# Kernel tuning notes

Hardware: AMD Instinct MI355X
Metric: run time of the kernel (lower is better)

Reference implementation:

```python
import jax, jax.numpy as jnp
import numpy as np

HIDDEN = 768
NUM_HEADS = 12
HEAD_DIM = HIDDEN // NUM_HEADS


def setup_inputs() -> dict:
    key = jax.random.key(0)
    ks = jax.random.split(key, 10)
    B, S = 4, 2048
    scale = 1.0 / np.sqrt(HIDDEN)
    inp = {
        "hidden_states": jax.random.normal(ks[0], (B, S, HIDDEN), dtype=jnp.float32),
        "attention_mask": jnp.ones((B, S), dtype=jnp.float32),
        "Wq": jax.random.normal(ks[1], (HIDDEN, HIDDEN), dtype=jnp.float32) * scale,
        "bq": jnp.zeros((HIDDEN,), dtype=jnp.float32),
        "Wk": jax.random.normal(ks[2], (HIDDEN, HIDDEN), dtype=jnp.float32) * scale,
        "bk": jnp.zeros((HIDDEN,), dtype=jnp.float32),
        "Wv": jax.random.normal(ks[3], (HIDDEN, HIDDEN), dtype=jnp.float32) * scale,
        "bv": jnp.zeros((HIDDEN,), dtype=jnp.float32),
        "Wo": jax.random.normal(ks[4], (HIDDEN, HIDDEN), dtype=jnp.float32) * scale,
        "bo": jnp.zeros((HIDDEN,), dtype=jnp.float32),
    }
    return inp


def _split_heads(x):
    # [B,S,H] -> [B,nh,S,dh]
    B, S, _ = x.shape
    return x.reshape(B, S, NUM_HEADS, HEAD_DIM).transpose(0, 2, 1, 3)


def reference(hidden_states, attention_mask, Wq, bq, Wk, bk, Wv, bv, Wo, bo):
    # Linear projections (torch nn.Linear: x @ W.T + b; here W stored as [in,out])
    q = _split_heads(hidden_states @ Wq + bq)
    k = _split_heads(hidden_states @ Wk + bk)
    v = _split_heads(hidden_states @ Wv + bv)

    # scores: [B,nh,S,S]
    scores = jnp.einsum("bhqd,bhkd->bhqk", q, k) / np.sqrt(HEAD_DIM).astype(np.float32)

    # outer-product mask: [B,1,S,S], broadcast over heads
    ext = (attention_mask[:, :, None] * attention_mask[:, None, :])[:, None, :, :]
    scores = ext * scores - (1.0 - ext) * 1e9

    probs = jax.nn.softmax(scores, axis=-1)
    ctx = jnp.einsum("bhqk,bhkd->bhqd", probs, v)  # [B,nh,S,dh]
    B, _, S, _ = ctx.shape
    ctx = ctx.transpose(0, 2, 1, 3).reshape(B, S, HIDDEN)
    out = ctx @ Wo + bo
    # torch F.gelu default: exact (erf-based)
    return jax.nn.gelu(out, approximate=False)
```

## Files before the change

### kernel.cpp

```cpp
#include <hip/hip_runtime.h>
#include <math.h>

#define HIDDEN 768
#define NH 12
#define DH 64
#define SEQ 2048
#define BATCH 4

typedef __bf16 bf16;
typedef bf16 bf16x4 __attribute__((ext_vector_type(4)));
typedef bf16 bf16x8 __attribute__((ext_vector_type(8)));
typedef float f32x4 __attribute__((ext_vector_type(4)));

__device__ __forceinline__ void load_lds16(const void* g, void* l) {
    __builtin_amdgcn_global_load_lds(
        (__attribute__((address_space(1))) void*)g,
        (__attribute__((address_space(3))) void*)l, 16, 0, 0);
}

__global__ __launch_bounds__(256) void prep_x(const float* __restrict__ X,
                                              bf16* __restrict__ Xb) {
    const size_t i = ((size_t)blockIdx.x * 256 + threadIdx.x) * 8;
    float4 a = *(const float4*)(X + i);
    float4 b = *(const float4*)(X + i + 4);
    bf16x8 o = {(bf16)a.x, (bf16)a.y, (bf16)a.z, (bf16)a.w,
                (bf16)b.x, (bf16)b.y, (bf16)b.z, (bf16)b.w};
    *(bf16x8*)(Xb + i) = o;
}

__global__ __launch_bounds__(256) void prep_w(const float* __restrict__ Wq,
                                              const float* __restrict__ Wk,
                                              const float* __restrict__ Wv,
                                              const float* __restrict__ Wo,
                                              bf16* __restrict__ Wt,
                                              bf16* __restrict__ Wot_hi,
                                              bf16* __restrict__ Wot_lo) {
    __shared__ float Ts[64][68];
    const int tid = threadIdx.x;
    const int n0 = blockIdx.x * 64, k0 = blockIdx.y * 64, z = blockIdx.z;
    const float* W = (z == 0) ? Wq : (z == 1) ? Wk : (z == 2) ? Wv : Wo;

    {
        const int r = tid >> 2, c = (tid & 3) << 4;
        const float* src = W + (size_t)(k0 + r) * HIDDEN + n0 + c;
#pragma unroll
        for (int j = 0; j < 4; ++j)
            *(float4*)&Ts[r][c + 4 * j] = *(const float4*)(src + 4 * j);
    }
    __syncthreads();

    const int nl = tid >> 2, kc = (tid & 3) << 4;
    float v[16];
#pragma unroll
    for (int j = 0; j < 16; ++j) v[j] = Ts[kc + j][nl];

    if (z < 3) {
        bf16 hi[16];
#pragma unroll
        for (int j = 0; j < 16; ++j) hi[j] = (bf16)v[j];
        const size_t off = (size_t)(z * HIDDEN + n0 + nl) * HIDDEN + k0 + kc;
        *(bf16x8*)(Wt + off) = *(bf16x8*)&hi[0];
        *(bf16x8*)(Wt + off + 8) = *(bf16x8*)&hi[8];
    } else {
        bf16 hi[16], lo[16];
#pragma unroll
        for (int j = 0; j < 16; ++j) {
            hi[j] = (bf16)v[j];
            lo[j] = (bf16)(v[j] - (float)hi[j]);
        }
        const size_t off = (size_t)(n0 + nl) * HIDDEN + k0 + kc;
        *(bf16x8*)(Wot_hi + off) = *(bf16x8*)&hi[0];
        *(bf16x8*)(Wot_hi + off + 8) = *(bf16x8*)&hi[8];
        *(bf16x8*)(Wot_lo + off) = *(bf16x8*)&lo[0];
        *(bf16x8*)(Wot_lo + off + 8) = *(bf16x8*)&lo[8];
    }
}

__global__ __launch_bounds__(256, 3) void gemm_qkv(
    const bf16* __restrict__ Xb, const bf16* __restrict__ Wt,
    const float* __restrict__ bq, const float* __restrict__ bk,
    const float* __restrict__ bv, bf16* __restrict__ q_out,
    bf16* __restrict__ k_out, bf16* __restrict__ v_out) {
    __shared__ bf16 As[128 * 64];
    __shared__ bf16 Bs[192 * 64];

    const int tid = threadIdx.x;
    const int ln = tid & 63, wv = tid >> 6;
    const int quad = ln >> 4, l16 = ln & 15;
    const int wm = wv >> 1, wn = wv & 1;
    const int n0 = blockIdx.x * 192, m0 = blockIdx.y * 128;

    f32x4 acc[4][6];
#pragma unroll
    for (int i = 0; i < 4; ++i)
#pragma unroll
        for (int j = 0; j < 6; ++j) acc[i][j] = (f32x4){0.f, 0.f, 0.f, 0.f};

    const int r8 = ln >> 3;
    const int bcol_sw = ((ln & 7) << 4) ^ (r8 << 4);
    const char* gA =
        (const char*)Xb + ((size_t)(m0 + wv * 32 + r8) * HIDDEN) * 2 + bcol_sw;
    const char* gB =
        (const char*)Wt + ((size_t)(n0 + wv * 48 + r8) * HIDDEN) * 2 + bcol_sw;
    bf16* As_w = As + (wv * 32) * 64;
    bf16* Bs_w = Bs + (wv * 48) * 64;

    const int fsw = (l16 & 7) << 4;

    for (int k0 = 0; k0 < HIDDEN; k0 += 64) {
        __syncthreads();
#pragma unroll
        for (int j = 0; j < 4; ++j)
            load_lds16(gA + (size_t)k0 * 2 + (size_t)j * (8 * HIDDEN * 2),
                       As_w + j * 8 * 64);
#pragma unroll
        for (int j = 0; j < 6; ++j)
            load_lds16(gB + (size_t)k0 * 2 + (size_t)j * (8 * HIDDEN * 2),
                       Bs_w + j * 8 * 64);
        __syncthreads();

#pragma unroll
        for (int kk = 0; kk < 2; ++kk) {
            const int kb = kk * 64;
            bf16x8 ah[4], bh[6];
#pragma unroll
            for (int i = 0; i < 4; ++i)
                ah[i] = *(const bf16x8*)((const char*)As +
                                         (wm * 64 + i * 16 + l16) * 128 +
                                         ((kb + quad * 16) ^ fsw));
#pragma unroll
            for (int i = 0; i < 6; ++i)
                bh[i] = *(const bf16x8*)((const char*)Bs +
                                         (wn * 96 + i * 16 + l16) * 128 +
                                         ((kb + quad * 16) ^ fsw));
#pragma unroll
            for (int mi = 0; mi < 4; ++mi)
#pragma unroll
                for (int ni = 0; ni < 6; ++ni)
                    acc[mi][ni] = __builtin_amdgcn_mfma_f32_16x16x32_bf16(
                        ah[mi], bh[ni], acc[mi][ni], 0, 0, 0);
        }
    }

    const int nb = n0 + wn * 96;
    const int which = nb / HIDDEN;
    const int nrel = nb - which * HIDDEN;

    if (which < 2) {
        const float scale = (which == 0) ? 0.18033688011112042f : 1.0f;
        const float* bias = (which == 0) ? bq : bk;
        bf16* dst = (which == 0) ? q_out : k_out;
#pragma unroll
        for (int ni = 0; ni < 6; ++ni) {
            const int nn = nrel + ni * 16;
            const int h = nn >> 6;
            const int dh = (nn & 63) + l16;
            const float bb = bias[nn + l16];
#pragma unroll
            for (int mi = 0; mi < 4; ++mi)
#pragma unroll
                for (int r = 0; r < 4; ++r) {
                    const int m = m0 + wm * 64 + mi * 16 + quad * 4 + r;
                    const int bi = m >> 11, s = m & (SEQ - 1);
                    dst[(((size_t)(bi * NH + h) * SEQ + s) << 6) + dh] =
                        (bf16)(scale * (acc[mi][ni][r] + bb));
                }
        }
    } else {
        const int bi = m0 >> 11;
        const int sbase = (m0 & (SEQ - 1)) + wm * 64;
#pragma unroll
        for (int ni = 0; ni < 6; ++ni) {
            const int nn = nrel + ni * 16;
            const int h = nn >> 6;
            const int dh = (nn & 63) + l16;
            const float bb = bv[nn + l16];
            bf16* vrow = v_out + ((size_t)(bi * NH + h) * DH + dh) * SEQ;
#pragma unroll
            for (int mi = 0; mi < 4; ++mi) {
                bf16x4 pk = {(bf16)(acc[mi][ni][0] + bb),
                             (bf16)(acc[mi][ni][1] + bb),
                             (bf16)(acc[mi][ni][2] + bb),
                             (bf16)(acc[mi][ni][3] + bb)};
                *(bf16x4*)(vrow + sbase + mi * 16 + quad * 4) = pk;
            }
        }
    }
}

__global__ __launch_bounds__(256) void attn_mfma(const bf16* __restrict__ Q,
                                                 const bf16* __restrict__ K,
                                                 const bf16* __restrict__ Vt,
                                                 const float* __restrict__ mask,
                                                 bf16* __restrict__ ctx_hi,
                                                 bf16* __restrict__ ctx_lo) {
    __shared__ bf16 Ks[64 * 64];
    __shared__ bf16 Vts[64 * 64];
    __shared__ bf16 Ps[128 * 64];
    __shared__ float Ms[SEQ];
    __shared__ int allones_s;

    const int tid = threadIdx.x;
    const int ln = tid & 63, w = tid >> 6;
    const int quad = ln >> 4, l16 = ln & 15;

    const int wg = blockIdx.x;
    const int logical = (wg & 7) * 96 + (wg >> 3);
    const int qt = logical & 15;
    const int h = (logical >> 4) % NH;
    const int b = logical / (16 * NH);

    const size_t bh = (size_t)b * NH + h;
    const bf16* Qp = Q + ((bh * SEQ + (size_t)qt * 128) << 6);
    const bf16* Kp = K + (bh * SEQ << 6);
    const bf16* Vp = Vt + (bh * DH) * SEQ;

    if (tid == 0) allones_s = 1;
    {
        float4 m0 = *(const float4*)(mask + (size_t)b * SEQ + tid * 8);
        float4 m1 = *(const float4*)(mask + (size_t)b * SEQ + tid * 8 + 4);
        *(float4*)&Ms[tid * 8] = m0;
        *(float4*)&Ms[tid * 8 + 4] = m1;
        bool ok = (m0.x == 1.f) & (m0.y == 1.f) & (m0.z == 1.f) &
                  (m0.w == 1.f) & (m1.x == 1.f) & (m1.y == 1.f) &
                  (m1.z == 1.f) & (m1.w == 1.f);
        __syncthreads();
        if (!ok) allones_s = 0;
    }
    __syncthreads();
    const bool fastmask = (allones_s != 0);

    bf16x8 qb[2][2];
#pragma unroll
    for (int qg = 0; qg < 2; ++qg)
#pragma unroll
        for (int hf = 0; hf < 2; ++hf)
            qb[qg][hf] = *(const bf16x8*)(Qp + ((w * 32 + qg * 16 + l16) << 6) +
                                          hf * 32 + quad * 8);
    float mq[2];
#pragma unroll
    for (int qg = 0; qg < 2; ++qg)
        mq[qg] = Ms[qt * 128 + w * 32 + qg * 16 + l16];

    float l_i[2] = {0.f, 0.f};
    f32x4 acc[4][2];
#pragma unroll
    for (int fd = 0; fd < 4; ++fd)
#pragma unroll
        for (int qg = 0; qg < 2; ++qg) acc[fd][qg] = (f32x4){0.f, 0.f, 0.f, 0.f};

    const int sr = tid >> 2, sc = (tid & 3) << 4;
    const int ssw = (sr & 7) << 3;
    const int d0 = sc ^ ssw, d1 = (sc + 8) ^ ssw;
    const bf16* kbase = Kp + ((size_t)sr << 6) + sc;
    const bf16* vbase = Vp + (size_t)sr * SEQ + sc;

    bf16x8 kr0, kr1, vr0, vr1;
    kr0 = *(const bf16x8*)kbase;
    kr1 = *(const bf16x8*)(kbase + 8);
    vr0 = *(const bf16x8*)vbase;
    vr1 = *(const bf16x8*)(vbase + 8);

    for (int kt = 0; kt < SEQ / 64; ++kt) {
        __syncthreads();
        *(bf16x8*)&Ks[sr * 64 + d0] = kr0;
        *(bf16x8*)&Ks[sr * 64 + d1] = kr1;
        *(bf16x8*)&Vts[sr * 64 + d0] = vr0;
        *(bf16x8*)&Vts[sr * 64 + d1] = vr1;
        __syncthreads();
        if (kt + 1 < SEQ / 64) {
            kr0 = *(const bf16x8*)(kbase + ((size_t)(kt + 1) << 12));
            kr1 = *(const bf16x8*)(kbase + ((size_t)(kt + 1) << 12) + 8);
            vr0 = *(const bf16x8*)(vbase + (kt + 1) * 64);
            vr1 = *(const bf16x8*)(vbase + (kt + 1) * 64 + 8);
        }

        const int fsw = (l16 & 7) << 3;
        f32x4 st[4][2];
#pragma unroll
        for (int f = 0; f < 4; ++f) {
            const int krow = (f * 16 + l16) * 64;
            bf16x8 ka0 = *(bf16x8*)&Ks[krow + ((quad * 8) ^ fsw)];
            bf16x8 ka1 = *(bf16x8*)&Ks[krow + ((32 + quad * 8) ^ fsw)];
#pragma unroll
            for (int qg = 0; qg < 2; ++qg) {
                f32x4 c = {0.f, 0.f, 0.f, 0.f};
                c = __builtin_amdgcn_mfma_f32_16x16x32_bf16(ka0, qb[qg][0], c, 0, 0, 0);
                c = __builtin_amdgcn_mfma_f32_16x16x32_bf16(ka1, qb[qg][1], c, 0, 0, 0);
                st[f][qg] = c;
            }
        }

        if (!fastmask) {
#pragma unroll
            for (int f = 0; f < 4; ++f) {
                const float4 mk4 = *(const float4*)&Ms[kt * 64 + f * 16 + quad * 4];
                const float mkk[4] = {mk4.x, mk4.y, mk4.z, mk4.w};
#pragma unroll
                for (int qg = 0; qg < 2; ++qg)
#pragma unroll
                    for (int r = 0; r < 4; ++r) {
                        const float ext = mq[qg] * mkk[r];
                        st[f][qg][r] =
                            ext * st[f][qg][r] - (1.0f - ext) * 1.4426950e9f;
                    }
            }
        }

#pragma unroll
        for (int qg = 0; qg < 2; ++qg) {
            const int row = w * 32 + qg * 16 + l16;
            const int sw = (row & 7) << 3;
            bf16* prow = &Ps[row * 64];
#pragma unroll
            for (int f = 0; f < 4; ++f) {
                float p0 = __builtin_amdgcn_exp2f(st[f][qg][0]);
                float p1 = __builtin_amdgcn_exp2f(st[f][qg][1]);
                float p2 = __builtin_amdgcn_exp2f(st[f][qg][2]);
                float p3 = __builtin_amdgcn_exp2f(st[f][qg][3]);
                l_i[qg] += (p0 + p1) + (p2 + p3);
                bf16x4 pk = {(bf16)p0, (bf16)p1, (bf16)p2, (bf16)p3};
                *(bf16x4*)&prow[(f * 16 + quad * 4) ^ sw] = pk;
            }
        }

        bf16x8 pb[2][2];
#pragma unroll
        for (int qg = 0; qg < 2; ++qg) {
            const int row = w * 32 + qg * 16 + l16;
            const int sw = (row & 7) << 3;
#pragma unroll
            for (int hf = 0; hf < 2; ++hf)
                pb[qg][hf] =
                    *(bf16x8*)&Ps[row * 64 + ((hf * 32 + quad * 8) ^ sw)];
        }
#pragma unroll
        for (int fd = 0; fd < 4; ++fd) {
            const int vrow = (fd * 16 + l16) * 64;
            bf16x8 va0 = *(bf16x8*)&Vts[vrow + ((quad * 8) ^ fsw)];
            bf16x8 va1 = *(bf16x8*)&Vts[vrow + ((32 + quad * 8) ^ fsw)];
#pragma unroll
            for (int qg = 0; qg < 2; ++qg) {
                f32x4 c = acc[fd][qg];
                c = __builtin_amdgcn_mfma_f32_16x16x32_bf16(va0, pb[qg][0], c, 0, 0, 0);
                c = __builtin_amdgcn_mfma_f32_16x16x32_bf16(va1, pb[qg][1], c, 0, 0, 0);
                acc[fd][qg] = c;
            }
        }
    }

#pragma unroll
    for (int qg = 0; qg < 2; ++qg) {
        l_i[qg] += __shfl_xor(l_i[qg], 16);
        l_i[qg] += __shfl_xor(l_i[qg], 32);
    }

#pragma unroll
    for (int qg = 0; qg < 2; ++qg) {
        const float inv = 1.0f / l_i[qg];
        const size_t row = (size_t)b * SEQ + qt * 128 + w * 32 + qg * 16 + l16;
#pragma unroll
        for (int fd = 0; fd < 4; ++fd) {
            bf16 hi[4], lo[4];
#pragma unroll
            for (int r = 0; r < 4; ++r) {
                const float o = acc[fd][qg][r] * inv;
                hi[r] = (bf16)o;
                lo[r] = (bf16)(o - (float)hi[r]);
            }
            const size_t off = row * HIDDEN + h * 64 + fd * 16 + quad * 4;
            *(bf16x4*)(ctx_hi + off) = *(bf16x4*)&hi[0];
            *(bf16x4*)(ctx_lo + off) = *(bf16x4*)&lo[0];
        }
    }
}

__global__ __launch_bounds__(256) void gemm_out(const bf16* __restrict__ Ah,
                                                const bf16* __restrict__ Al,
                                                const bf16* __restrict__ Bhi,
                                                const bf16* __restrict__ Blo,
                                                const float* __restrict__ bo,
                                                float* __restrict__ fout) {
    __shared__ bf16 As_hi[128 * 64];
    __shared__ bf16 As_lo[128 * 64];
    __shared__ bf16 Bs_hi[64 * 64];
    __shared__ bf16 Bs_lo[64 * 64];

    const int tid = threadIdx.x;
    const int ln = tid & 63, wv = tid >> 6;
    const int quad = ln >> 4, l16 = ln & 15;
    const int wm = wv >> 1, wn = wv & 1;
    const int n0 = blockIdx.x * 64, m0 = blockIdx.y * 128;

    f32x4 acc[4][2];
#pragma unroll
    for (int i = 0; i < 4; ++i)
#pragma unroll
        for (int j = 0; j < 2; ++j) acc[i][j] = (f32x4){0.f, 0.f, 0.f, 0.f};

    const int r8 = ln >> 3;
    const int bcol_sw = ((ln & 7) << 4) ^ (r8 << 4);
    const char* gAh =
        (const char*)Ah + ((size_t)(m0 + wv * 32 + r8) * HIDDEN) * 2 + bcol_sw;
    const char* gAl =
        (const char*)Al + ((size_t)(m0 + wv * 32 + r8) * HIDDEN) * 2 + bcol_sw;
    const char* gBh =
        (const char*)Bhi + ((size_t)(n0 + wv * 16 + r8) * HIDDEN) * 2 + bcol_sw;
    const char* gBl =
        (const char*)Blo + ((size_t)(n0 + wv * 16 + r8) * HIDDEN) * 2 + bcol_sw;
    bf16* Ash_w = As_hi + (wv * 32) * 64;
    bf16* Asl_w = As_lo + (wv * 32) * 64;
    bf16* Bsh_w = Bs_hi + (wv * 16) * 64;
    bf16* Bsl_w = Bs_lo + (wv * 16) * 64;

    const int fsw = (l16 & 7) << 4;

    for (int k0 = 0; k0 < HIDDEN; k0 += 64) {
        __syncthreads();
#pragma unroll
        for (int j = 0; j < 4; ++j) {
            load_lds16(gAh + (size_t)k0 * 2 + (size_t)j * (8 * HIDDEN * 2),
                       Ash_w + j * 8 * 64);
            load_lds16(gAl + (size_t)k0 * 2 + (size_t)j * (8 * HIDDEN * 2),
                       Asl_w + j * 8 * 64);
        }
#pragma unroll
        for (int j = 0; j < 2; ++j) {
            load_lds16(gBh + (size_t)k0 * 2 + (size_t)j * (8 * HIDDEN * 2),
                       Bsh_w + j * 8 * 64);
            load_lds16(gBl + (size_t)k0 * 2 + (size_t)j * (8 * HIDDEN * 2),
                       Bsl_w + j * 8 * 64);
        }
        __syncthreads();

#pragma unroll
        for (int kk = 0; kk < 2; ++kk) {
            const int kb = kk * 64;
            bf16x8 ah[4], al[4], bh[2], bl[2];
#pragma unroll
            for (int i = 0; i < 4; ++i) {
                const int row = (wm * 64 + i * 16 + l16) * 128;
                ah[i] = *(const bf16x8*)((const char*)As_hi + row +
                                         ((kb + quad * 16) ^ fsw));
                al[i] = *(const bf16x8*)((const char*)As_lo + row +
                                         ((kb + quad * 16) ^ fsw));
            }
#pragma unroll
            for (int i = 0; i < 2; ++i) {
                const int row = (wn * 32 + i * 16 + l16) * 128;
                bh[i] = *(const bf16x8*)((const char*)Bs_hi + row +
                                         ((kb + quad * 16) ^ fsw));
                bl[i] = *(const bf16x8*)((const char*)Bs_lo + row +
                                         ((kb + quad * 16) ^ fsw));
            }
#pragma unroll
            for (int mi = 0; mi < 4; ++mi)
#pragma unroll
                for (int ni = 0; ni < 2; ++ni) {
                    f32x4 c = acc[mi][ni];
                    c = __builtin_amdgcn_mfma_f32_16x16x32_bf16(ah[mi], bh[ni],
                                                                c, 0, 0, 0);
                    c = __builtin_amdgcn_mfma_f32_16x16x32_bf16(ah[mi], bl[ni],
                                                                c, 0, 0, 0);
                    c = __builtin_amdgcn_mfma_f32_16x16x32_bf16(al[mi], bh[ni],
                                                                c, 0, 0, 0);
                    acc[mi][ni] = c;
                }
        }
    }

#pragma unroll
    for (int ni = 0; ni < 2; ++ni) {
        const int n = n0 + wn * 32 + ni * 16 + l16;
        const float bb = bo[n];
#pragma unroll
        for (int mi = 0; mi < 4; ++mi)
#pragma unroll
            for (int r = 0; r < 4; ++r) {
                const int m = m0 + wm * 64 + mi * 16 + quad * 4 + r;
                float x = acc[mi][ni][r] + bb;
                x = 0.5f * x * (1.0f + erff(x * 0.70710678118654752440f));
                fout[(size_t)m * HIDDEN + n] = x;
            }
    }
}

extern "C" void kernel_launch(void* const* d_in, const int* in_sizes, int n_in,
                              void* d_out, int out_size, void* d_ws, size_t ws_size,
                              hipStream_t stream) {
    const float* X    = (const float*)d_in[0];
    const float* mask = (const float*)d_in[1];
    const float* Wq   = (const float*)d_in[2];
    const float* bq   = (const float*)d_in[3];
    const float* Wk   = (const float*)d_in[4];
    const float* bk   = (const float*)d_in[5];
    const float* Wv   = (const float*)d_in[6];
    const float* bv   = (const float*)d_in[7];
    const float* Wo   = (const float*)d_in[8];
    const float* bo   = (const float*)d_in[9];
    float* out = (float*)d_out;

    char* w = (char*)d_ws;
    const size_t NE = (size_t)BATCH * SEQ * HIDDEN;
    bf16* q_ws   = (bf16*)w;  w += NE * 2;
    bf16* k_ws   = (bf16*)w;  w += NE * 2;
    bf16* vt_ws  = (bf16*)w;  w += NE * 2;
    bf16* ctx_hi = (bf16*)w;  w += NE * 2;
    bf16* ctx_lo = (bf16*)w;  w += NE * 2;
    bf16* Xb     = (bf16*)w;  w += NE * 2;
    bf16* Wt     = (bf16*)w;  w += (size_t)3 * HIDDEN * HIDDEN * 2;
    bf16* Wot_hi = (bf16*)w;  w += (size_t)HIDDEN * HIDDEN * 2;
    bf16* Wot_lo = (bf16*)w;  w += (size_t)HIDDEN * HIDDEN * 2;

    prep_x<<<(int)(NE / 2048), 256, 0, stream>>>(X, Xb);
    prep_w<<<dim3(12, 12, 4), 256, 0, stream>>>(Wq, Wk, Wv, Wo, Wt, Wot_hi,
                                                Wot_lo);
    gemm_qkv<<<dim3(12, 64), 256, 0, stream>>>(Xb, Wt, bq, bk, bv, q_ws, k_ws,
                                               vt_ws);
    attn_mfma<<<dim3(16 * NH * BATCH), 256, 0, stream>>>(
        q_ws, k_ws, vt_ws, mask, ctx_hi, ctx_lo);
    gemm_out<<<dim3(12, 64), 256, 0, stream>>>(ctx_hi, ctx_lo, Wot_hi, Wot_lo,
                                               bo, out);
}
```

Baseline: 261.4 us.

## Merge prep kernels and remap GEMM blocks for XCD-local L2 reuse

The separate X-cast and weight-transpose kernels become one launch, with the block ID range deciding which job a block does, saving one launch and its gap. Both GEMMs now use a flat 1D grid and remap block IDs so that blocks landing on the same XCD (round-robin by ID mod 8) work on neighbouring M rows and share all N tiles. The aim is better L2 reuse of A rows within each XCD's private L2. The remapping relies on the hardware dispatching blocks round-robin across XCDs.

Result: faster. 251.3 us (-3.9%).

```diff
diff --git a/kernel.cpp b/kernel.cpp
--- a/kernel.cpp
+++ b/kernel.cpp
@@ -18,34 +18,38 @@
         (__attribute__((address_space(3))) void*)l, 16, 0, 0);
 }
 
-__global__ __launch_bounds__(256) void prep_x(const float* __restrict__ X,
-                                              bf16* __restrict__ Xb) {
-    const size_t i = ((size_t)blockIdx.x * 256 + threadIdx.x) * 8;
-    float4 a = *(const float4*)(X + i);
-    float4 b = *(const float4*)(X + i + 4);
-    bf16x8 o = {(bf16)a.x, (bf16)a.y, (bf16)a.z, (bf16)a.w,
-                (bf16)b.x, (bf16)b.y, (bf16)b.z, (bf16)b.w};
-    *(bf16x8*)(Xb + i) = o;
-}
-
-__global__ __launch_bounds__(256) void prep_w(const float* __restrict__ Wq,
-                                              const float* __restrict__ Wk,
-                                              const float* __restrict__ Wv,
-                                              const float* __restrict__ Wo,
-                                              bf16* __restrict__ Wt,
-                                              bf16* __restrict__ Wot_hi,
-                                              bf16* __restrict__ Wot_lo) {
+__global__ __launch_bounds__(256) void prep_xw(
+    const float* __restrict__ X, bf16* __restrict__ Xb,
+    const float* __restrict__ Wq, const float* __restrict__ Wk,
+    const float* __restrict__ Wv, const float* __restrict__ Wo,
+    bf16* __restrict__ Wt, bf16* __restrict__ Wot_hi,
+    bf16* __restrict__ Wot_lo) {
+    const int bid = blockIdx.x;
+    const int tid = threadIdx.x;
+
+    if (bid < 3072) {
+        const size_t i = ((size_t)bid * 256 + tid) * 8;
+        float4 a = *(const float4*)(X + i);
+        float4 b = *(const float4*)(X + i + 4);
+        bf16x8 o = {(bf16)a.x, (bf16)a.y, (bf16)a.z, (bf16)a.w,
+                    (bf16)b.x, (bf16)b.y, (bf16)b.z, (bf16)b.w};
+        *(bf16x8*)(Xb + i) = o;
+        return;
+    }
+
     __shared__ float Ts[64][68];
-    const int tid = threadIdx.x;
-    const int n0 = blockIdx.x * 64, k0 = blockIdx.y * 64, z = blockIdx.z;
+    const int r = bid - 3072;
+    const int z = r / 144;
+    const int rem = r - z * 144;
+    const int n0 = (rem % 12) * 64, k0 = (rem / 12) * 64;
     const float* W = (z == 0) ? Wq : (z == 1) ? Wk : (z == 2) ? Wv : Wo;
 
     {
-        const int r = tid >> 2, c = (tid & 3) << 4;
-        const float* src = W + (size_t)(k0 + r) * HIDDEN + n0 + c;
+        const int rr = tid >> 2, c = (tid & 3) << 4;
+        const float* src = W + (size_t)(k0 + rr) * HIDDEN + n0 + c;
 #pragma unroll
         for (int j = 0; j < 4; ++j)
-            *(float4*)&Ts[r][c + 4 * j] = *(const float4*)(src + 4 * j);
+            *(float4*)&Ts[rr][c + 4 * j] = *(const float4*)(src + 4 * j);
     }
     __syncthreads();
 
@@ -88,7 +92,11 @@
     const int ln = tid & 63, wv = tid >> 6;
     const int quad = ln >> 4, l16 = ln & 15;
     const int wm = wv >> 1, wn = wv & 1;
-    const int n0 = blockIdx.x * 192, m0 = blockIdx.y * 128;
+
+    const int wg = blockIdx.x;
+    const int xcd = wg & 7, i6 = wg >> 3;
+    const int n0 = (i6 % 12) * 192;
+    const int m0 = (xcd * 8 + i6 / 12) * 128;
 
     f32x4 acc[4][6];
 #pragma unroll
@@ -390,7 +398,11 @@
     const int ln = tid & 63, wv = tid >> 6;
     const int quad = ln >> 4, l16 = ln & 15;
     const int wm = wv >> 1, wn = wv & 1;
-    const int n0 = blockIdx.x * 64, m0 = blockIdx.y * 128;
+
+    const int wg = blockIdx.x;
+    const int xcd = wg & 7, i6 = wg >> 3;
+    const int n0 = (i6 % 12) * 64;
+    const int m0 = (xcd * 8 + i6 / 12) * 128;
 
     f32x4 acc[4][2];
 #pragma unroll
@@ -512,13 +524,12 @@
     bf16* Wot_hi = (bf16*)w;  w += (size_t)HIDDEN * HIDDEN * 2;
     bf16* Wot_lo = (bf16*)w;  w += (size_t)HIDDEN * HIDDEN * 2;
 
-    prep_x<<<(int)(NE / 2048), 256, 0, stream>>>(X, Xb);
-    prep_w<<<dim3(12, 12, 4), 256, 0, stream>>>(Wq, Wk, Wv, Wo, Wt, Wot_hi,
-                                                Wot_lo);
-    gemm_qkv<<<dim3(12, 64), 256, 0, stream>>>(Xb, Wt, bq, bk, bv, q_ws, k_ws,
-                                               vt_ws);
+    prep_xw<<<3648, 256, 0, stream>>>(X, Xb, Wq, Wk, Wv, Wo, Wt, Wot_hi,
+                                      Wot_lo);
+    gemm_qkv<<<dim3(768), 256, 0, stream>>>(Xb, Wt, bq, bk, bv, q_ws, k_ws,
+                                            vt_ws);
     attn_mfma<<<dim3(16 * NH * BATCH), 256, 0, stream>>>(
         q_ws, k_ws, vt_ws, mask, ctx_hi, ctx_lo);
-    gemm_out<<<dim3(12, 64), 256, 0, stream>>>(ctx_hi, ctx_lo, Wot_hi, Wot_lo,
-                                               bo, out);
+    gemm_out<<<dim3(768), 256, 0, stream>>>(ctx_hi, ctx_lo, Wot_hi, Wot_lo,
+                                            bo, out);
 }
```
